# Optimization experiments

Measured on AMD Instinct MI355X. Metric: run time of the kernel, lower is better.

The kernel has to match this reference:

```python
import jax, jax.numpy as jnp
import numpy as np

N = 50000      # nodes
E = 1600000    # edges (avg degree 32)
D_IN = 128
HID = 64


def setup_inputs() -> dict:
    key = jax.random.key(0)
    ks = jax.random.split(key, 7)
    x = jax.random.normal(ks[0], (N, D_IN), dtype=jnp.float32)
    ei = jax.random.randint(ks[1], (2, E), 0, N, dtype=jnp.int32)
    ew = jax.random.uniform(ks[2], (E,), dtype=jnp.float32)
    # GCNConv linear weights (glorot-ish scale); lin has no bias, conv bias added post-aggregation
    W1 = jax.random.normal(ks[3], (HID, D_IN), dtype=jnp.float32) * (1.0 / np.sqrt(D_IN))
    b1 = jnp.zeros((HID,), dtype=jnp.float32)
    W2 = jax.random.normal(ks[4], (HID, HID), dtype=jnp.float32) * (1.0 / np.sqrt(HID))
    b2 = jnp.zeros((HID,), dtype=jnp.float32)
    return {"x": x, "ei": ei, "ew": ew, "W1": W1, "b1": b1, "W2": W2, "b2": b2}


def _gcn_conv(x, src, dst, ew_all, W, b, n_nodes):
    """PyG GCNConv: gcn_norm (self-loops already appended) + x@W.T, gather-scale-scatter, +b."""
    deg = jax.ops.segment_sum(ew_all, dst, num_segments=n_nodes)  # dst-side weighted degree
    dinv = jnp.where(deg > 0, jax.lax.rsqrt(deg), 0.0)            # deg^{-1/2}, inf->0
    norm = dinv[src] * ew_all * dinv[dst]                          # [E+N]
    h = x @ W.T                                                    # [N, hid]
    msg = h[src] * norm[:, None]                                   # gather + scale
    out = jax.ops.segment_sum(msg, dst, num_segments=n_nodes)     # scatter-add
    return out + b


def reference(x, ei, ew, W1, b1, W2, b2):
    n_nodes = x.shape[0]
    # add self loops once (fill value 1.0), shared by both conv layers
    loop = jnp.arange(n_nodes, dtype=ei.dtype)
    src = jnp.concatenate([ei[0], loop])
    dst = jnp.concatenate([ei[1], loop])
    ew_all = jnp.concatenate([ew, jnp.ones((n_nodes,), dtype=ew.dtype)])

    h1 = jax.nn.relu(_gcn_conv(x, src, dst, ew_all, W1, b1, n_nodes))
    # dropout is identity in eval mode
    h2 = _gcn_conv(h1, src, dst, ew_all, W2, b2, n_nodes)
    return h2 + h1
```

## Files before the change

### kernel.cpp

```cpp
#include <hip/hip_runtime.h>

#define HID 64
#define DIN 128
#define NBLK 512
#define CSH 14
#define CAP (1 << CSH)

typedef unsigned long long ull;
typedef unsigned short u16;

static __device__ __forceinline__ u16 f2bf(float f) {
  unsigned u = __float_as_uint(f);
  unsigned lsb = (u >> 16) & 1u;
  u += 0x7fffu + lsb;
  return (u16)(u >> 16);
}


__global__ __launch_bounds__(512) void k_build(const int* __restrict__ src,
                                               const int* __restrict__ dst,
                                               const float* __restrict__ ew,
                                               int* __restrict__ cursor,
                                               int2* __restrict__ bufA,
                                               int E, int NBC, int chunk,
                                               const float* __restrict__ W1,
                                               const float* __restrict__ W2,
                                               float* __restrict__ WT1,
                                               float* __restrict__ WT2) {
  int b = blockIdx.x, tid = threadIdx.x;
  if (b >= NBLK) {
    int idx = (b - NBLK) * 512 + tid;
    if (idx < DIN * 64) {
      int d = idx >> 6, j = idx & 63;
      WT1[idx] = W1[j * DIN + d];
    }
    int i2 = idx - DIN * 64;
    if (i2 >= 0 && i2 < HID * 64) {
      int d = i2 >> 6, j = i2 & 63;
      WT2[i2] = W2[j * HID + d];
    }
    return;
  }
  __shared__ int h[256];
  __shared__ int cur[256];
  if (tid < 256) h[tid] = 0;
  __syncthreads();
  int e0 = b * chunk, e1 = min(E, e0 + chunk);
  for (int e = e0 + tid; e < e1; e += 512) atomicAdd(&h[dst[e] >> 8], 1);
  __syncthreads();
  if (tid < 256) {
    int c = h[tid];
    int ofs = (c > 0) ? atomicAdd(&cursor[tid], c) : 0;
    cur[tid] = (tid << CSH) + ofs;
  }
  __syncthreads();
  for (int e = e0 + tid; e < e1; e += 512) {
    int s = src[e], d = dst[e];
    float w = ew[e];
    int p = atomicAdd(&cur[d >> 8], 1);
    bufA[p] = make_int2(__float_as_int(w), (int)(((unsigned)s << 16) | (unsigned)d));
  }
}


__global__ __launch_bounds__(1024) void k_passB(const int2* __restrict__ bufA,
                                                const int* __restrict__ cursor,
                                                int2* __restrict__ bufB,
                                                int* __restrict__ offs,
                                                int* __restrict__ cnt,
                                                float* __restrict__ dinv,
                                                int NBC, int N) {
  int bin = blockIdx.x, tid = threadIdx.x;
  __shared__ int h2[256];
  __shared__ int cur[256];
  __shared__ float dg[256];
  int bbase = bin << CSH;
  int m = cursor[bin];
  if (tid < 256) { h2[tid] = 0; dg[tid] = 0.f; }
  __syncthreads();
  int2 rloc[16];
#pragma unroll
  for (int k = 0; k < 16; ++k) {
    int i = tid + k * 1024;
    if (i < m) {
      rloc[k] = bufA[bbase + i];
      atomicAdd(&h2[(unsigned)rloc[k].y & 255u], 1);
    }
  }
  __syncthreads();
  int own = (tid < 256) ? h2[tid] : 0;
  for (int o = 1; o < 256; o <<= 1) {
    int u = 0;
    if (tid < 256 && tid >= o) u = h2[tid - o];
    __syncthreads();
    if (tid < 256) h2[tid] += u;
    __syncthreads();
  }
  int nd = (bin << 8) + tid;
  if (tid < 256) {
    int excl = h2[tid] - own;
    cur[tid] = excl;
    if (nd < N) { offs[nd] = bbase + excl; cnt[nd] = own; }
  }
  __syncthreads();
#pragma unroll
  for (int k = 0; k < 16; ++k) {
    int i = tid + k * 1024;
    if (i < m) {
      int2 r = rloc[k];
      unsigned sd = (unsigned)r.y;
      int dl = (int)(sd & 255u);
      int p = atomicAdd(&cur[dl], 1);
      bufB[bbase + p] = make_int2(r.x, (int)(sd >> 16));
      atomicAdd(&dg[dl], __int_as_float(r.x));
    }
  }
  __syncthreads();
  if (tid < 256 && nd < N) dinv[nd] = rsqrtf(1.0f + dg[tid]);
}


template <int K>
__global__ __launch_bounds__(256) void k_gemm(const float* __restrict__ X,
                                              const float* __restrict__ WTg,
                                              const float* __restrict__ dinv,
                                              u16* __restrict__ out, int n_nodes) {
  constexpr int PAD = 68;
  __shared__ float XT[64 * PAD];
  __shared__ float WL[64 * PAD];
  const int tid = threadIdx.x;
  const int n0 = blockIdx.x * 64;
  const int tx = tid & 15;
  const int ty = tid >> 4;
  float acc[4][4] = {{0.f}};

  for (int ph = 0; ph < K / 64; ++ph) {
    const int d0 = ph * 64;
    __syncthreads();
#pragma unroll
    for (int k = 0; k < 4; ++k) {
      int f = tid + k * 256;
      int r = f >> 4, q = f & 15;
      int n = n0 + r;
      float4 xv = (n < n_nodes)
        ? *reinterpret_cast<const float4*>(&X[(size_t)n * K + d0 + 4 * q])
        : make_float4(0.f, 0.f, 0.f, 0.f);
      *reinterpret_cast<float4*>(&XT[r * PAD + 4 * q]) = xv;
      float4 wv = *reinterpret_cast<const float4*>(&WTg[(size_t)(d0 + r) * 64 + 4 * q]);
      *reinterpret_cast<float4*>(&WL[r * PAD + 4 * q]) = wv;
    }
    __syncthreads();
#pragma unroll 4
    for (int dd = 0; dd < 64; dd += 4) {
      float4 xs[4], ws[4];
#pragma unroll
      for (int mi = 0; mi < 4; ++mi)
        xs[mi] = *reinterpret_cast<const float4*>(&XT[(4 * ty + mi) * PAD + dd]);
#pragma unroll
      for (int dk = 0; dk < 4; ++dk)
        ws[dk] = *reinterpret_cast<const float4*>(&WL[(dd + dk) * PAD + 4 * tx]);
#pragma unroll
      for (int mi = 0; mi < 4; ++mi) {
        float xm[4] = {xs[mi].x, xs[mi].y, xs[mi].z, xs[mi].w};
#pragma unroll
        for (int dk = 0; dk < 4; ++dk) {
          acc[mi][0] = fmaf(xm[dk], ws[dk].x, acc[mi][0]);
          acc[mi][1] = fmaf(xm[dk], ws[dk].y, acc[mi][1]);
          acc[mi][2] = fmaf(xm[dk], ws[dk].z, acc[mi][2]);
          acc[mi][3] = fmaf(xm[dk], ws[dk].w, acc[mi][3]);
        }
      }
    }
  }

#pragma unroll
  for (int mi = 0; mi < 4; ++mi) {
    int n = n0 + 4 * ty + mi;
    if (n < n_nodes) {
      float dn = dinv[n];
      ushort4 o = make_ushort4(f2bf(acc[mi][0] * dn), f2bf(acc[mi][1] * dn),
                               f2bf(acc[mi][2] * dn), f2bf(acc[mi][3] * dn));
      *reinterpret_cast<ushort4*>(&out[(size_t)n * HID + 4 * tx]) = o;
    }
  }
}


__device__ __forceinline__ void bfma8(const uint4& v, float w, float* a) {
  a[0] = fmaf(__uint_as_float(v.x << 16), w, a[0]);
  a[1] = fmaf(__uint_as_float(v.x & 0xffff0000u), w, a[1]);
  a[2] = fmaf(__uint_as_float(v.y << 16), w, a[2]);
  a[3] = fmaf(__uint_as_float(v.y & 0xffff0000u), w, a[3]);
  a[4] = fmaf(__uint_as_float(v.z << 16), w, a[4]);
  a[5] = fmaf(__uint_as_float(v.z & 0xffff0000u), w, a[5]);
  a[6] = fmaf(__uint_as_float(v.w << 16), w, a[6]);
  a[7] = fmaf(__uint_as_float(v.w & 0xffff0000u), w, a[7]);
}

__global__ __launch_bounds__(256) void k_agg(const u16* __restrict__ h,
                                             const int2* __restrict__ recs,
                                             const int* __restrict__ offs,
                                             const int* __restrict__ cnt,
                                             const float* __restrict__ dinv,
                                             const float* __restrict__ bias,
                                             const float* __restrict__ resid,
                                             float* __restrict__ out, int n_nodes, int mode) {
  int tid = threadIdx.x;
  int lane = tid & 63;
  int g = lane >> 3;
  int p8 = (lane & 7) * 8;
  int node = (blockIdx.x * 4 + (tid >> 6)) * 8 + g;
  if (node >= n_nodes) return;
  int beg = offs[node], end = beg + cnt[node];
  float di = dinv[node];

  float a[8], b[8];
  {
    uint4 v = *reinterpret_cast<const uint4*>(&h[(size_t)node * HID + p8]);
    a[0] = __uint_as_float(v.x << 16);
    a[1] = __uint_as_float(v.x & 0xffff0000u);
    a[2] = __uint_as_float(v.y << 16);
    a[3] = __uint_as_float(v.y & 0xffff0000u);
    a[4] = __uint_as_float(v.z << 16);
    a[5] = __uint_as_float(v.z & 0xffff0000u);
    a[6] = __uint_as_float(v.w << 16);
    a[7] = __uint_as_float(v.w & 0xffff0000u);
#pragma unroll
    for (int j = 0; j < 8; ++j) b[j] = 0.f;
  }

  const int gb = lane & 56;
  int i = beg;
  while (i + 8 <= end) {
    ull rr = *reinterpret_cast<const ull*>(&recs[i + (lane & 7)]);
#pragma unroll
    for (int k = 0; k < 8; ++k) {
      ull q = __shfl(rr, gb | k, 64);
      float wk = __uint_as_float((unsigned)q);
      int sk = (int)(q >> 32);
      uint4 vk = *reinterpret_cast<const uint4*>(&h[(size_t)sk * HID + p8]);
      bfma8(vk, wk, (k & 1) ? b : a);
    }
    i += 8;
  }
  if (i + 4 <= end) {
    int2 r0 = recs[i];     int2 r1 = recs[i + 1];
    int2 r2 = recs[i + 2]; int2 r3 = recs[i + 3];
    uint4 v0 = *reinterpret_cast<const uint4*>(&h[(size_t)r0.y * HID + p8]);
    uint4 v1 = *reinterpret_cast<const uint4*>(&h[(size_t)r1.y * HID + p8]);
    uint4 v2 = *reinterpret_cast<const uint4*>(&h[(size_t)r2.y * HID + p8]);
    uint4 v3 = *reinterpret_cast<const uint4*>(&h[(size_t)r3.y * HID + p8]);
    bfma8(v0, __int_as_float(r0.x), a);
    bfma8(v1, __int_as_float(r1.x), b);
    bfma8(v2, __int_as_float(r2.x), a);
    bfma8(v3, __int_as_float(r3.x), b);
    i += 4;
  }
  if (i + 2 <= end) {
    int2 r0 = recs[i];     int2 r1 = recs[i + 1];
    uint4 v0 = *reinterpret_cast<const uint4*>(&h[(size_t)r0.y * HID + p8]);
    uint4 v1 = *reinterpret_cast<const uint4*>(&h[(size_t)r1.y * HID + p8]);
    bfma8(v0, __int_as_float(r0.x), a);
    bfma8(v1, __int_as_float(r1.x), b);
    i += 2;
  }
  if (i < end) {
    int2 r0 = recs[i];
    uint4 v0 = *reinterpret_cast<const uint4*>(&h[(size_t)r0.y * HID + p8]);
    bfma8(v0, __int_as_float(r0.x), a);
  }

  float r[8];
#pragma unroll
  for (int j = 0; j < 8; ++j) r[j] = (a[j] + b[j]) * di;
  float4 bb0 = *reinterpret_cast<const float4*>(&bias[p8]);
  float4 bb1 = *reinterpret_cast<const float4*>(&bias[p8 + 4]);
  r[0] += bb0.x; r[1] += bb0.y; r[2] += bb0.z; r[3] += bb0.w;
  r[4] += bb1.x; r[5] += bb1.y; r[6] += bb1.z; r[7] += bb1.w;
  if (mode == 0) {
#pragma unroll
    for (int j = 0; j < 8; ++j) r[j] = fmaxf(r[j], 0.f);
  } else {
    float4 rs0 = *reinterpret_cast<const float4*>(&resid[(size_t)node * HID + p8]);
    float4 rs1 = *reinterpret_cast<const float4*>(&resid[(size_t)node * HID + p8 + 4]);
    r[0] += rs0.x; r[1] += rs0.y; r[2] += rs0.z; r[3] += rs0.w;
    r[4] += rs1.x; r[5] += rs1.y; r[6] += rs1.z; r[7] += rs1.w;
  }
  *reinterpret_cast<float4*>(&out[(size_t)node * HID + p8]) =
      make_float4(r[0], r[1], r[2], r[3]);
  *reinterpret_cast<float4*>(&out[(size_t)node * HID + p8 + 4]) =
      make_float4(r[4], r[5], r[6], r[7]);
}


extern "C" void kernel_launch(void* const* d_in, const int* in_sizes, int n_in,
                              void* d_out, int out_size, void* d_ws, size_t ws_size,
                              hipStream_t stream) {
  const float* x  = (const float*)d_in[0];
  const int*   ei = (const int*)d_in[1];
  const float* ew = (const float*)d_in[2];
  const float* W1 = (const float*)d_in[3];
  const float* b1 = (const float*)d_in[4];
  const float* W2 = (const float*)d_in[5];
  const float* b2 = (const float*)d_in[6];
  float* out = (float*)d_out;

  const int N = in_sizes[0] / DIN;
  const int E = in_sizes[2];
  const int* src = ei;
  const int* dst = ei + E;

  const int NBC = (N + 255) >> 8;
  const int chunk = (E + NBLK - 1) / NBLK;
  const int nslab = NBC << CSH;

  char* p = (char*)d_ws;
  auto carve = [&](size_t bytes) {
    char* r = p;
    p += (bytes + 255) & ~(size_t)255;
    return r;
  };
  int*   cursor = (int*)carve(256 * 4);
  int*   offs   = (int*)carve((size_t)N * 4);
  int*   cnt    = (int*)carve((size_t)N * 4);
  float* dinv   = (float*)carve((size_t)N * 4);
  int2*  bufA   = (int2*)carve((size_t)nslab * 8);
  int2*  bufB   = (int2*)carve((size_t)nslab * 8);
  u16*   h      = (u16*)carve((size_t)N * HID * 2);
  float* h1     = (float*)carve((size_t)N * HID * 4);
  float* WT1    = (float*)carve((size_t)DIN * HID * 4);
  float* WT2    = (float*)carve((size_t)HID * HID * 4);

  int gblk = (N + 63) / 64;
  int ablk = (N + 31) / 32;
  int tblk = ((DIN + HID) * 64 + 511) / 512;

  hipMemsetAsync(cursor, 0, 256 * 4, stream);
  k_build<<<NBLK + tblk, 512, 0, stream>>>(src, dst, ew, cursor, bufA, E, NBC, chunk,
                                           W1, W2, WT1, WT2);
  k_passB<<<NBC, 1024, 0, stream>>>(bufA, cursor, bufB, offs, cnt, dinv, NBC, N);

  k_gemm<DIN><<<gblk, 256, 0, stream>>>(x, WT1, dinv, h, N);
  k_agg<<<ablk, 256, 0, stream>>>(h, bufB, offs, cnt, dinv, b1, nullptr, h1, N, 0);
  k_gemm<HID><<<gblk, 256, 0, stream>>>(h1, WT2, dinv, h, N);
  k_agg<<<ablk, 256, 0, stream>>>(h, bufB, offs, cnt, dinv, b2, h1, out, N, 1);
}
```

Before: 221.8 us.

## Fuse layer-1 GEMM into graph build and layer-2 GEMM into aggregation

The first GEMM now runs on extra blocks of the edge-bucketing kernel, so it overlaps graph construction. It no longer uses dinv, and the weight transpose happens in shared memory. The dinv[src] scaling moves into aggregation, which now gathers dinv per edge. The first aggregation is fused with the second GEMM through a shared-memory tile of h1, cutting two launches and one global round trip. The cost is extra per-edge dinv loads and heavier 512-thread blocks with more shared memory, which may lower occupancy.

```diff
diff --git a/kernel.cpp b/kernel.cpp
--- a/kernel.cpp
+++ b/kernel.cpp
@@ -5,6 +5,7 @@
 #define NBLK 512
 #define CSH 14
 #define CAP (1 << CSH)
+#define PAD 68
 
 typedef unsigned long long ull;
 typedef unsigned short u16;
@@ -17,39 +18,103 @@
 }
 
 
-__global__ __launch_bounds__(512) void k_build(const int* __restrict__ src,
-                                               const int* __restrict__ dst,
-                                               const float* __restrict__ ew,
-                                               int* __restrict__ cursor,
-                                               int2* __restrict__ bufA,
-                                               int E, int NBC, int chunk,
-                                               const float* __restrict__ W1,
-                                               const float* __restrict__ W2,
-                                               float* __restrict__ WT1,
-                                               float* __restrict__ WT2) {
+template <int K, bool XT_PRELOADED>
+__device__ __forceinline__ void gemm_tile(const float* __restrict__ X,
+                                          const float* __restrict__ W,
+                                          u16* __restrict__ out,
+                                          float* XT, float* WL,
+                                          int n0, int n_nodes, int tid) {
+  const int tx = tid & 15;
+  const int ty = tid >> 4;
+  float acc[2][4] = {{0.f}};
+
+  for (int ph = 0; ph < K / 64; ++ph) {
+    const int d0 = ph * 64;
+    __syncthreads();
+    if (!XT_PRELOADED) {
+#pragma unroll
+      for (int k = 0; k < 2; ++k) {
+        int f = tid + k * 512;
+        int r = f >> 4, q = f & 15;
+        int n = n0 + r;
+        float4 xv = (n < n_nodes)
+          ? *reinterpret_cast<const float4*>(&X[(size_t)n * K + d0 + 4 * q])
+          : make_float4(0.f, 0.f, 0.f, 0.f);
+        *reinterpret_cast<float4*>(&XT[r * PAD + 4 * q]) = xv;
+      }
+    }
+#pragma unroll
+    for (int k = 0; k < 2; ++k) {
+      int gq = tid + k * 512;
+      int j = gq >> 4, qd = gq & 15;
+      float4 wv = *reinterpret_cast<const float4*>(&W[(size_t)j * K + d0 + 4 * qd]);
+      WL[(4 * qd + 0) * PAD + j] = wv.x;
+      WL[(4 * qd + 1) * PAD + j] = wv.y;
+      WL[(4 * qd + 2) * PAD + j] = wv.z;
+      WL[(4 * qd + 3) * PAD + j] = wv.w;
+    }
+    __syncthreads();
+#pragma unroll 4
+    for (int dd = 0; dd < 64; dd += 4) {
+      float4 ws[4];
+#pragma unroll
+      for (int dk = 0; dk < 4; ++dk)
+        ws[dk] = *reinterpret_cast<const float4*>(&WL[(dd + dk) * PAD + 4 * tx]);
+      float4 x0 = *reinterpret_cast<const float4*>(&XT[ty * PAD + dd]);
+      float4 x1 = *reinterpret_cast<const float4*>(&XT[(ty + 32) * PAD + dd]);
+      float xm0[4] = {x0.x, x0.y, x0.z, x0.w};
+      float xm1[4] = {x1.x, x1.y, x1.z, x1.w};
+#pragma unroll
+      for (int dk = 0; dk < 4; ++dk) {
+        acc[0][0] = fmaf(xm0[dk], ws[dk].x, acc[0][0]);
+        acc[0][1] = fmaf(xm0[dk], ws[dk].y, acc[0][1]);
+        acc[0][2] = fmaf(xm0[dk], ws[dk].z, acc[0][2]);
+        acc[0][3] = fmaf(xm0[dk], ws[dk].w, acc[0][3]);
+        acc[1][0] = fmaf(xm1[dk], ws[dk].x, acc[1][0]);
+        acc[1][1] = fmaf(xm1[dk], ws[dk].y, acc[1][1]);
+        acc[1][2] = fmaf(xm1[dk], ws[dk].z, acc[1][2]);
+        acc[1][3] = fmaf(xm1[dk], ws[dk].w, acc[1][3]);
+      }
+    }
+  }
+
+#pragma unroll
+  for (int mi = 0; mi < 2; ++mi) {
+    int n = n0 + mi * 32 + ty;
+    if (n < n_nodes) {
+      ushort4 o = make_ushort4(f2bf(acc[mi][0]), f2bf(acc[mi][1]),
+                               f2bf(acc[mi][2]), f2bf(acc[mi][3]));
+      *reinterpret_cast<ushort4*>(&out[(size_t)n * HID + 4 * tx]) = o;
+    }
+  }
+}
+
+
+__global__ __launch_bounds__(512) void k_build_gemm(const int* __restrict__ src,
+                                                    const int* __restrict__ dst,
+                                                    const float* __restrict__ ew,
+                                                    int* __restrict__ cursor,
+                                                    int2* __restrict__ bufA,
+                                                    int E, int chunk,
+                                                    const float* __restrict__ x,
+                                                    const float* __restrict__ W1,
+                                                    u16* __restrict__ h,
+                                                    int n_nodes) {
+  __shared__ float S[2 * 64 * PAD];
   int b = blockIdx.x, tid = threadIdx.x;
   if (b >= NBLK) {
-    int idx = (b - NBLK) * 512 + tid;
-    if (idx < DIN * 64) {
-      int d = idx >> 6, j = idx & 63;
-      WT1[idx] = W1[j * DIN + d];
-    }
-    int i2 = idx - DIN * 64;
-    if (i2 >= 0 && i2 < HID * 64) {
-      int d = i2 >> 6, j = i2 & 63;
-      WT2[i2] = W2[j * HID + d];
-    }
+    gemm_tile<DIN, false>(x, W1, h, S, S + 64 * PAD, (b - NBLK) * 64, n_nodes, tid);
     return;
   }
-  __shared__ int h[256];
-  __shared__ int cur[256];
-  if (tid < 256) h[tid] = 0;
+  int* hst = (int*)S;
+  int* cur = (int*)S + 256;
+  if (tid < 256) hst[tid] = 0;
   __syncthreads();
   int e0 = b * chunk, e1 = min(E, e0 + chunk);
-  for (int e = e0 + tid; e < e1; e += 512) atomicAdd(&h[dst[e] >> 8], 1);
+  for (int e = e0 + tid; e < e1; e += 512) atomicAdd(&hst[dst[e] >> 8], 1);
   __syncthreads();
   if (tid < 256) {
-    int c = h[tid];
+    int c = hst[tid];
     int ofs = (c > 0) ? atomicAdd(&cursor[tid], c) : 0;
     cur[tid] = (tid << CSH) + ofs;
   }
@@ -120,72 +185,6 @@
 }
 
 
-template <int K>
-__global__ __launch_bounds__(256) void k_gemm(const float* __restrict__ X,
-                                              const float* __restrict__ WTg,
-                                              const float* __restrict__ dinv,
-                                              u16* __restrict__ out, int n_nodes) {
-  constexpr int PAD = 68;
-  __shared__ float XT[64 * PAD];
-  __shared__ float WL[64 * PAD];
-  const int tid = threadIdx.x;
-  const int n0 = blockIdx.x * 64;
-  const int tx = tid & 15;
-  const int ty = tid >> 4;
-  float acc[4][4] = {{0.f}};
-
-  for (int ph = 0; ph < K / 64; ++ph) {
-    const int d0 = ph * 64;
-    __syncthreads();
-#pragma unroll
-    for (int k = 0; k < 4; ++k) {
-      int f = tid + k * 256;
-      int r = f >> 4, q = f & 15;
-      int n = n0 + r;
-      float4 xv = (n < n_nodes)
-        ? *reinterpret_cast<const float4*>(&X[(size_t)n * K + d0 + 4 * q])
-        : make_float4(0.f, 0.f, 0.f, 0.f);
-      *reinterpret_cast<float4*>(&XT[r * PAD + 4 * q]) = xv;
-      float4 wv = *reinterpret_cast<const float4*>(&WTg[(size_t)(d0 + r) * 64 + 4 * q]);
-      *reinterpret_cast<float4*>(&WL[r * PAD + 4 * q]) = wv;
-    }
-    __syncthreads();
-#pragma unroll 4
-    for (int dd = 0; dd < 64; dd += 4) {
-      float4 xs[4], ws[4];
-#pragma unroll
-      for (int mi = 0; mi < 4; ++mi)
-        xs[mi] = *reinterpret_cast<const float4*>(&XT[(4 * ty + mi) * PAD + dd]);
-#pragma unroll
-      for (int dk = 0; dk < 4; ++dk)
-        ws[dk] = *reinterpret_cast<const float4*>(&WL[(dd + dk) * PAD + 4 * tx]);
-#pragma unroll
-      for (int mi = 0; mi < 4; ++mi) {
-        float xm[4] = {xs[mi].x, xs[mi].y, xs[mi].z, xs[mi].w};
-#pragma unroll
-        for (int dk = 0; dk < 4; ++dk) {
-          acc[mi][0] = fmaf(xm[dk], ws[dk].x, acc[mi][0]);
-          acc[mi][1] = fmaf(xm[dk], ws[dk].y, acc[mi][1]);
-          acc[mi][2] = fmaf(xm[dk], ws[dk].z, acc[mi][2]);
-          acc[mi][3] = fmaf(xm[dk], ws[dk].w, acc[mi][3]);
-        }
-      }
-    }
-  }
-
-#pragma unroll
-  for (int mi = 0; mi < 4; ++mi) {
-    int n = n0 + 4 * ty + mi;
-    if (n < n_nodes) {
-      float dn = dinv[n];
-      ushort4 o = make_ushort4(f2bf(acc[mi][0] * dn), f2bf(acc[mi][1] * dn),
-                               f2bf(acc[mi][2] * dn), f2bf(acc[mi][3] * dn));
-      *reinterpret_cast<ushort4*>(&out[(size_t)n * HID + 4 * tx]) = o;
-    }
-  }
-}
-
-
 __device__ __forceinline__ void bfma8(const uint4& v, float w, float* a) {
   a[0] = fmaf(__uint_as_float(v.x << 16), w, a[0]);
   a[1] = fmaf(__uint_as_float(v.x & 0xffff0000u), w, a[1]);
@@ -197,34 +196,22 @@
   a[7] = fmaf(__uint_as_float(v.w & 0xffff0000u), w, a[7]);
 }
 
-__global__ __launch_bounds__(256) void k_agg(const u16* __restrict__ h,
-                                             const int2* __restrict__ recs,
-                                             const int* __restrict__ offs,
-                                             const int* __restrict__ cnt,
-                                             const float* __restrict__ dinv,
-                                             const float* __restrict__ bias,
-                                             const float* __restrict__ resid,
-                                             float* __restrict__ out, int n_nodes, int mode) {
-  int tid = threadIdx.x;
-  int lane = tid & 63;
-  int g = lane >> 3;
-  int p8 = (lane & 7) * 8;
-  int node = (blockIdx.x * 4 + (tid >> 6)) * 8 + g;
-  if (node >= n_nodes) return;
-  int beg = offs[node], end = beg + cnt[node];
-  float di = dinv[node];
-
+__device__ __forceinline__ void agg_node(const u16* __restrict__ h,
+                                         const int2* __restrict__ recs,
+                                         const float* __restrict__ dinv,
+                                         int beg, int end, int node, float di,
+                                         int lane, int p8, float* r) {
   float a[8], b[8];
   {
     uint4 v = *reinterpret_cast<const uint4*>(&h[(size_t)node * HID + p8]);
-    a[0] = __uint_as_float(v.x << 16);
-    a[1] = __uint_as_float(v.x & 0xffff0000u);
-    a[2] = __uint_as_float(v.y << 16);
-    a[3] = __uint_as_float(v.y & 0xffff0000u);
-    a[4] = __uint_as_float(v.z << 16);
-    a[5] = __uint_as_float(v.z & 0xffff0000u);
-    a[6] = __uint_as_float(v.w << 16);
-    a[7] = __uint_as_float(v.w & 0xffff0000u);
+    a[0] = __uint_as_float(v.x << 16) * di;
+    a[1] = __uint_as_float(v.x & 0xffff0000u) * di;
+    a[2] = __uint_as_float(v.y << 16) * di;
+    a[3] = __uint_as_float(v.y & 0xffff0000u) * di;
+    a[4] = __uint_as_float(v.z << 16) * di;
+    a[5] = __uint_as_float(v.z & 0xffff0000u) * di;
+    a[6] = __uint_as_float(v.w << 16) * di;
+    a[7] = __uint_as_float(v.w & 0xffff0000u) * di;
 #pragma unroll
     for (int j = 0; j < 8; ++j) b[j] = 0.f;
   }
@@ -233,6 +220,8 @@
   int i = beg;
   while (i + 8 <= end) {
     ull rr = *reinterpret_cast<const ull*>(&recs[i + (lane & 7)]);
+    float wd = __uint_as_float((unsigned)rr) * dinv[(int)(rr >> 32)];
+    rr = (rr & 0xffffffff00000000ull) | (ull)__float_as_uint(wd);
 #pragma unroll
     for (int k = 0; k < 8; ++k) {
       ull q = __shfl(rr, gb | k, 64);
@@ -250,42 +239,95 @@
     uint4 v1 = *reinterpret_cast<const uint4*>(&h[(size_t)r1.y * HID + p8]);
     uint4 v2 = *reinterpret_cast<const uint4*>(&h[(size_t)r2.y * HID + p8]);
     uint4 v3 = *reinterpret_cast<const uint4*>(&h[(size_t)r3.y * HID + p8]);
-    bfma8(v0, __int_as_float(r0.x), a);
-    bfma8(v1, __int_as_float(r1.x), b);
-    bfma8(v2, __int_as_float(r2.x), a);
-    bfma8(v3, __int_as_float(r3.x), b);
+    bfma8(v0, __int_as_float(r0.x) * dinv[r0.y], a);
+    bfma8(v1, __int_as_float(r1.x) * dinv[r1.y], b);
+    bfma8(v2, __int_as_float(r2.x) * dinv[r2.y], a);
+    bfma8(v3, __int_as_float(r3.x) * dinv[r3.y], b);
     i += 4;
   }
   if (i + 2 <= end) {
     int2 r0 = recs[i];     int2 r1 = recs[i + 1];
     uint4 v0 = *reinterpret_cast<const uint4*>(&h[(size_t)r0.y * HID + p8]);
     uint4 v1 = *reinterpret_cast<const uint4*>(&h[(size_t)r1.y * HID + p8]);
-    bfma8(v0, __int_as_float(r0.x), a);
-    bfma8(v1, __int_as_float(r1.x), b);
+    bfma8(v0, __int_as_float(r0.x) * dinv[r0.y], a);
+    bfma8(v1, __int_as_float(r1.x) * dinv[r1.y], b);
     i += 2;
   }
   if (i < end) {
     int2 r0 = recs[i];
     uint4 v0 = *reinterpret_cast<const uint4*>(&h[(size_t)r0.y * HID + p8]);
-    bfma8(v0, __int_as_float(r0.x), a);
-  }
-
+    bfma8(v0, __int_as_float(r0.x) * dinv[r0.y], a);
+  }
+#pragma unroll
+  for (int j = 0; j < 8; ++j) r[j] = (a[j] + b[j]) * di;
+}
+
+
+__global__ __launch_bounds__(512) void k_agg_gemm(const u16* __restrict__ h,
+                                                  const int2* __restrict__ recs,
+                                                  const int* __restrict__ offs,
+                                                  const int* __restrict__ cnt,
+                                                  const float* __restrict__ dinv,
+                                                  const float* __restrict__ bias,
+                                                  const float* __restrict__ W2,
+                                                  float* __restrict__ h1,
+                                                  u16* __restrict__ h2,
+                                                  int n_nodes) {
+  __shared__ float S[2 * 64 * PAD];
+  float* XT = S;
+  float* WL = S + 64 * PAD;
+  int tid = threadIdx.x;
+  int lane = tid & 63;
+  int p8 = (lane & 7) * 8;
+  int nl = (tid >> 6) * 8 + (lane >> 3);
+  int node = blockIdx.x * 64 + nl;
+  if (node < n_nodes) {
+    float di = dinv[node];
+    float r[8];
+    agg_node(h, recs, dinv, offs[node], offs[node] + cnt[node], node, di,
+             lane, p8, r);
+    float4 bb0 = *reinterpret_cast<const float4*>(&bias[p8]);
+    float4 bb1 = *reinterpret_cast<const float4*>(&bias[p8 + 4]);
+    r[0] += bb0.x; r[1] += bb0.y; r[2] += bb0.z; r[3] += bb0.w;
+    r[4] += bb1.x; r[5] += bb1.y; r[6] += bb1.z; r[7] += bb1.w;
+#pragma unroll
+    for (int j = 0; j < 8; ++j) r[j] = fmaxf(r[j], 0.f);
+    float4 lo = make_float4(r[0], r[1], r[2], r[3]);
+    float4 hi = make_float4(r[4], r[5], r[6], r[7]);
+    *reinterpret_cast<float4*>(&h1[(size_t)node * HID + p8]) = lo;
+    *reinterpret_cast<float4*>(&h1[(size_t)node * HID + p8 + 4]) = hi;
+    *reinterpret_cast<float4*>(&XT[nl * PAD + p8]) = lo;
+    *reinterpret_cast<float4*>(&XT[nl * PAD + p8 + 4]) = hi;
+  }
+  gemm_tile<HID, true>(nullptr, W2, h2, XT, WL, blockIdx.x * 64, n_nodes, tid);
+}
+
+
+__global__ __launch_bounds__(256) void k_agg2(const u16* __restrict__ h,
+                                              const int2* __restrict__ recs,
+                                              const int* __restrict__ offs,
+                                              const int* __restrict__ cnt,
+                                              const float* __restrict__ dinv,
+                                              const float* __restrict__ bias,
+                                              const float* __restrict__ resid,
+                                              float* __restrict__ out, int n_nodes) {
+  int tid = threadIdx.x;
+  int lane = tid & 63;
+  int p8 = (lane & 7) * 8;
+  int node = (blockIdx.x * 4 + (tid >> 6)) * 8 + (lane >> 3);
+  if (node >= n_nodes) return;
+  float di = dinv[node];
   float r[8];
-#pragma unroll
-  for (int j = 0; j < 8; ++j) r[j] = (a[j] + b[j]) * di;
+  agg_node(h, recs, dinv, offs[node], offs[node] + cnt[node], node, di,
+           lane, p8, r);
   float4 bb0 = *reinterpret_cast<const float4*>(&bias[p8]);
   float4 bb1 = *reinterpret_cast<const float4*>(&bias[p8 + 4]);
-  r[0] += bb0.x; r[1] += bb0.y; r[2] += bb0.z; r[3] += bb0.w;
-  r[4] += bb1.x; r[5] += bb1.y; r[6] += bb1.z; r[7] += bb1.w;
-  if (mode == 0) {
-#pragma unroll
-    for (int j = 0; j < 8; ++j) r[j] = fmaxf(r[j], 0.f);
-  } else {
-    float4 rs0 = *reinterpret_cast<const float4*>(&resid[(size_t)node * HID + p8]);
-    float4 rs1 = *reinterpret_cast<const float4*>(&resid[(size_t)node * HID + p8 + 4]);
-    r[0] += rs0.x; r[1] += rs0.y; r[2] += rs0.z; r[3] += rs0.w;
-    r[4] += rs1.x; r[5] += rs1.y; r[6] += rs1.z; r[7] += rs1.w;
-  }
+  float4 rs0 = *reinterpret_cast<const float4*>(&resid[(size_t)node * HID + p8]);
+  float4 rs1 = *reinterpret_cast<const float4*>(&resid[(size_t)node * HID + p8 + 4]);
+  r[0] += bb0.x + rs0.x; r[1] += bb0.y + rs0.y;
+  r[2] += bb0.z + rs0.z; r[3] += bb0.w + rs0.w;
+  r[4] += bb1.x + rs1.x; r[5] += bb1.y + rs1.y;
+  r[6] += bb1.z + rs1.z; r[7] += bb1.w + rs1.w;
   *reinterpret_cast<float4*>(&out[(size_t)node * HID + p8]) =
       make_float4(r[0], r[1], r[2], r[3]);
   *reinterpret_cast<float4*>(&out[(size_t)node * HID + p8 + 4]) =
@@ -327,21 +369,16 @@
   int2*  bufA   = (int2*)carve((size_t)nslab * 8);
   int2*  bufB   = (int2*)carve((size_t)nslab * 8);
   u16*   h      = (u16*)carve((size_t)N * HID * 2);
+  u16*   h2     = (u16*)carve((size_t)N * HID * 2);
   float* h1     = (float*)carve((size_t)N * HID * 4);
-  float* WT1    = (float*)carve((size_t)DIN * HID * 4);
-  float* WT2    = (float*)carve((size_t)HID * HID * 4);
 
   int gblk = (N + 63) / 64;
   int ablk = (N + 31) / 32;
-  int tblk = ((DIN + HID) * 64 + 511) / 512;
 
   hipMemsetAsync(cursor, 0, 256 * 4, stream);
-  k_build<<<NBLK + tblk, 512, 0, stream>>>(src, dst, ew, cursor, bufA, E, NBC, chunk,
-                                           W1, W2, WT1, WT2);
+  k_build_gemm<<<NBLK + gblk, 512, 0, stream>>>(src, dst, ew, cursor, bufA, E, chunk,
+                                                x, W1, h, N);
   k_passB<<<NBC, 1024, 0, stream>>>(bufA, cursor, bufB, offs, cnt, dinv, NBC, N);
-
-  k_gemm<DIN><<<gblk, 256, 0, stream>>>(x, WT1, dinv, h, N);
-  k_agg<<<ablk, 256, 0, stream>>>(h, bufB, offs, cnt, dinv, b1, nullptr, h1, N, 0);
-  k_gemm<HID><<<gblk, 256, 0, stream>>>(h1, WT2, dinv, h, N);
-  k_agg<<<ablk, 256, 0, stream>>>(h, bufB, offs, cnt, dinv, b2, h1, out, N, 1);
-}
+  k_agg_gemm<<<gblk, 512, 0, stream>>>(h, bufB, offs, cnt, dinv, b1, W2, h1, h2, N);
+  k_agg2<<<ablk, 256, 0, stream>>>(h2, bufB, offs, cnt, dinv, b2, h1, out, N);
+}
```

New measurement: 216.1 us. 2.6% less time.
